# Optimization experiments

Measured on AMD Instinct MI355X. Metric: run time of the kernel, lower is better.

Reference implementation:

```python
import jax, jax.numpy as jnp
import numpy as np

B, S, D = 8, 2048, 1024

def setup_inputs() -> dict:
    key = jax.random.key(0)
    kq, kk, kv = jax.random.split(key, 3)
    qm = jax.random.normal(kq, (B, S, D), dtype=jnp.float32)
    km = jax.random.normal(kk, (B, S, D), dtype=jnp.float32)
    vm = jax.random.normal(kv, (B, S, D), dtype=jnp.float32)
    return {"qm": qm, "km": km, "vm": vm}

def reference(qm, km, vm):
    # qkm = qm @ km^T / sqrt(d_k)   -> [B, S, S]
    scale = 1.0 / jnp.sqrt(jnp.asarray(qm.shape[-1], dtype=qm.dtype))
    qkm = jnp.einsum('bqd,bkd->bqk', qm, km) * scale
    # NOTE: faithful to source: softmax is applied AFTER the second matmul,
    # i.e. softmax((QK^T/sqrt(d)) @ V, axis=-1). masking=False (module default).
    out = jnp.einsum('bqk,bkd->bqd', qkm, vm)  # [B, S, D]
    return jax.nn.softmax(out, axis=-1)
```

## Files before the change

### kernel.cpp

```cpp
#include <hip/hip_runtime.h>
#include <hip/hip_bf16.h>
#include <stdint.h>

#define BATCH 8
#define SEQ   2048
#define DIM   1024

typedef unsigned short u16;
typedef __attribute__((ext_vector_type(8))) short short8;
typedef __attribute__((ext_vector_type(4))) float f32x4;
typedef __attribute__((ext_vector_type(4))) unsigned short us4;

__device__ __forceinline__ u16 f2bf(float x){
  union { float f; uint32_t u; } c; c.f = x;
  uint32_t u = c.u;
  uint32_t r = u + 0x7fffu + ((u >> 16) & 1u);
  return (u16)(r >> 16);
}
__device__ __forceinline__ float bf2f(u16 s){
  union { uint32_t u; float f; } c; c.u = ((uint32_t)s) << 16;
  return c.f;
}

__device__ __forceinline__ void gload16(const void* g, void* l){
  __builtin_amdgcn_global_load_lds(
      (const __attribute__((address_space(1))) void*)g,
      (__attribute__((address_space(3))) void*)l, 16, 0, 0);
}

__global__ __launch_bounds__(256) void k_split(const float* __restrict__ src,
                                               u16* __restrict__ dst, int nchunk){
  for (int i = blockIdx.x*blockDim.x + threadIdx.x; i < nchunk; i += gridDim.x*blockDim.x){
    int r = i >> 8;
    int c = (i & 255) << 2;
    f32x4 v = *(const f32x4*)(src + (size_t)r*DIM + c);
    us4 h, l;
    #pragma unroll
    for (int j = 0; j < 4; j++){
      u16 hh = f2bf(v[j]);
      h[j] = hh;
      l[j] = f2bf(v[j] - bf2f(hh));
    }
    u16* d = dst + (size_t)r*(2*DIM) + c;
    *(us4*)d         = h;
    *(us4*)(d + DIM) = l;
  }
}

__global__ __launch_bounds__(256) void k_convert_kv(const float* __restrict__ K,
                                                    const float* __restrict__ V,
                                                    u16* __restrict__ Kt,
                                                    u16* __restrict__ Vt){
  __shared__ float tile[64][65];
  int z = blockIdx.z;
  const float* Src = (z < 8 ? K : V);
  u16* Dst = (z < 8 ? Kt : Vt);
  int zb = z & 7;
  const float* Vb = Src + (size_t)zb * SEQ * DIM;
  u16* Vtb = Dst + (size_t)zb * DIM * (2*SEQ);
  int s0 = blockIdx.x * 64, d0 = blockIdx.y * 64;
  int t = threadIdx.x;
  int rs = t >> 4;
  int cd = (t & 15) * 4;
  #pragma unroll
  for (int i = 0; i < 4; i++){
    int s = rs + i*16;
    f32x4 v = *(const f32x4*)(Vb + (size_t)(s0 + s)*DIM + d0 + cd);
    tile[s][cd+0] = v[0]; tile[s][cd+1] = v[1];
    tile[s][cd+2] = v[2]; tile[s][cd+3] = v[3];
  }
  __syncthreads();
  int dl = t >> 4;
  int sl = (t & 15) * 4;
  #pragma unroll
  for (int i = 0; i < 4; i++){
    int d = dl + i*16;
    us4 h, l;
    #pragma unroll
    for (int j = 0; j < 4; j++){
      float x = tile[sl+j][d];
      u16 hh = f2bf(x);
      h[j] = hh;
      l[j] = f2bf(x - bf2f(hh));
    }
    size_t off = (size_t)(d0 + d) * (2*SEQ) + s0 + sl;
    *(us4*)(Vtb + off)       = h;
    *(us4*)(Vtb + off + SEQ) = l;
  }
}

template<int KROW, int SPLITK, int TPZX, int TPZY>
__global__ __launch_bounds__(512,1) void k_gemm8(const u16* __restrict__ A,
                                                 const u16* __restrict__ B,
                                                 float* __restrict__ C,
                                                 size_t aStride, size_t bStride, size_t cStride){
  constexpr int LA = 2*KROW;
  constexpr int NT = 1024/32;
  __shared__ __align__(16) u16 lds[2][4][256*32];

  int xcd = blockIdx.x & 7;
  int idx = blockIdx.x >> 3;
  int nPerX = gridDim.x >> 3;
  int gid = xcd * nPerX + idx;
  constexpr int TPZ = TPZX*TPZY;
  int z  = gid / TPZ;
  int rm = gid % TPZ;
  int bx = rm % TPZX;
  int by = rm / TPZX;

  int zb = SPLITK ? (z & 7) : z;
  int kh = SPLITK ? (z >> 3) : 0;

  const u16* Ab = A + (size_t)zb * aStride + (size_t)kh * 1024;
  const u16* Bb = B + (size_t)zb * bStride + (size_t)kh * 1024;
  float* Cb = C + (size_t)z * cStride;

  int t0 = threadIdx.x, lane = t0 & 63, wv = t0 >> 6;
  int wm = (wv >> 2) * 128, wn = (wv & 3) * 64;
  int fr = lane & 15;
  int rdSlot = ((lane >> 4) ^ ((fr >> 1) & 3)) * 8;
  int srow = lane >> 2;
  int srcSlot = ((lane & 3) ^ ((lane >> 3) & 3)) * 8;

  const u16* aB = Ab + ((size_t)bx*256) * LA + srcSlot;
  const u16* bB = Bb + ((size_t)by*256) * LA + srcSlot;
  int ldsB0 = wv*512;

  f32x4 acc[8][4] = {};
  short8 fah[4], fal[4], fbh0[2], fbl0[2], fbh1[2], fbl1[2];

  #define STAGE8(buf, t32)                                                    \
    { _Pragma("unroll")                                                       \
      for (int hf = 0; hf < 2; hf++){                                         \
        size_t ro = (size_t)(wv*16 + hf*128 + srow) * LA + (size_t)(t32)*32;  \
        const u16* ga = aB + ro;                                              \
        const u16* gb = bB + ro;                                              \
        int lo = ldsB0 + hf*4096;                                             \
        gload16(ga,        &lds[buf][0][lo]);                                 \
        gload16(ga + KROW, &lds[buf][1][lo]);                                 \
        gload16(gb,        &lds[buf][2][lo]);                                 \
        gload16(gb + KROW, &lds[buf][3][lo]);                                 \
      } }

  #define LOAD_A(buf, h)                                                      \
    { _Pragma("unroll")                                                       \
      for (int q = 0; q < 4; q++){                                            \
        int ra = (wm + ((h)*4+q)*16 + fr)*32 + rdSlot;                        \
        fah[q] = *(const short8*)&lds[buf][0][ra];                            \
        fal[q] = *(const short8*)&lds[buf][1][ra];                            \
      } }
  #define LOAD_B0(buf)                                                        \
    { _Pragma("unroll")                                                       \
      for (int q = 0; q < 2; q++){                                            \
        int rb = (wn + q*16 + fr)*32 + rdSlot;                                \
        fbh0[q] = *(const short8*)&lds[buf][2][rb];                           \
        fbl0[q] = *(const short8*)&lds[buf][3][rb];                           \
      } }
  #define LOAD_B1(buf)                                                        \
    { _Pragma("unroll")                                                       \
      for (int q = 0; q < 2; q++){                                            \
        int rb = (wn + (2+q)*16 + fr)*32 + rdSlot;                            \
        fbh1[q] = *(const short8*)&lds[buf][2][rb];                           \
        fbl1[q] = *(const short8*)&lds[buf][3][rb];                           \
      } }

  #define MFMA_Q(h, bh, bl, nb)                                               \
    { _Pragma("unroll")                                                       \
      for (int q = 0; q < 4; q++){                                            \
        _Pragma("unroll")                                                     \
        for (int j = 0; j < 2; j++){                                          \
          f32x4 a0 = acc[(h)*4+q][(nb)+j];                                    \
          a0 = __builtin_amdgcn_mfma_f32_16x16x32_bf16(fah[q], bh[j], a0, 0,0,0); \
          a0 = __builtin_amdgcn_mfma_f32_16x16x32_bf16(fah[q], bl[j], a0, 0,0,0); \
          a0 = __builtin_amdgcn_mfma_f32_16x16x32_bf16(fal[q], bh[j], a0, 0,0,0); \
          acc[(h)*4+q][(nb)+j] = a0;                                          \
        } } }

  #define BARR()  __builtin_amdgcn_s_barrier()
  #define LGKM0() { asm volatile("s_waitcnt lgkmcnt(0)" ::: "memory"); __builtin_amdgcn_sched_barrier(0); }
  #define VMC0()  { asm volatile("s_waitcnt vmcnt(0)" ::: "memory"); __builtin_amdgcn_sched_barrier(0); }

  STAGE8(0, 0)
  VMC0()
  BARR();

  for (int t = 0; t < NT; t++){
    int buf = t & 1;
    if (t+1 < NT) STAGE8(buf^1, t+1)
    LOAD_A(buf, 0) LOAD_B0(buf)
    BARR(); LGKM0()
    __builtin_amdgcn_s_setprio(1); MFMA_Q(0, fbh0, fbl0, 0) __builtin_amdgcn_s_setprio(0);
    BARR();
    LOAD_B1(buf)
    BARR(); LGKM0()
    __builtin_amdgcn_s_setprio(1); MFMA_Q(0, fbh1, fbl1, 2) __builtin_amdgcn_s_setprio(0);
    BARR();
    LOAD_A(buf, 1)
    BARR(); LGKM0()
    __builtin_amdgcn_s_setprio(1); MFMA_Q(1, fbh1, fbl1, 2) __builtin_amdgcn_s_setprio(0);
    BARR();
    __builtin_amdgcn_s_setprio(1); MFMA_Q(1, fbh0, fbl0, 0) __builtin_amdgcn_s_setprio(0);
    if (t+1 < NT) VMC0()
    BARR();
  }

  #undef STAGE8
  #undef LOAD_A
  #undef LOAD_B0
  #undef LOAD_B1
  #undef MFMA_Q
  #undef BARR
  #undef LGKM0
  #undef VMC0

  int cr = (lane >> 4) * 4;
  #pragma unroll
  for (int mi = 0; mi < 8; mi++){
    int gr = bx*256 + wm + mi*16 + cr;
    #pragma unroll
    for (int ni = 0; ni < 4; ni++){
      int gc = by*256 + wn + ni*16 + fr;
      #pragma unroll
      for (int e = 0; e < 4; e++)
        Cb[(size_t)(gr + e) * 1024 + gc] = acc[mi][ni][e];
    }
  }
}

__global__ __launch_bounds__(256) void k_reduce_split(const float* __restrict__ P,
                                                      u16* __restrict__ Ws){
  int i = blockIdx.x*256 + threadIdx.x;
  int rg = i >> 8;
  int c  = (i & 255) * 4;
  f32x4 a = *(const f32x4*)(P + (size_t)rg*1024 + c);
  f32x4 b = *(const f32x4*)(P + ((size_t)rg + 8192)*1024 + c);
  us4 h, l;
  #pragma unroll
  for (int j = 0; j < 4; j++){
    float x = (a[j] + b[j]) * 0.03125f;
    u16 hh = f2bf(x);
    h[j] = hh;
    l[j] = f2bf(x - bf2f(hh));
  }
  int zb = rg >> 10, d = rg & 1023;
  u16* Wb = Ws + (size_t)zb * ((size_t)DIM * 2*DIM);
  *(us4*)(Wb + (size_t)d*2048 + c)        = h;
  *(us4*)(Wb + (size_t)d*2048 + 1024 + c) = l;
}

template<int N_, int KB, int SPLITOUT, int BX, int RX, int RY>
__global__ __launch_bounds__(256,2) void k_gemm2ph(const u16* __restrict__ A,
                                                   const u16* __restrict__ B,
                                                   void* __restrict__ Cout,
                                                   size_t aStride, size_t bStride, size_t cStride){
  constexpr int LA = 2*KB;
  __shared__ __align__(16) u16 lds[2][4][128*32];

  int orig = blockIdx.x;
  int xcd = orig & 7;
  int idx = orig >> 3;
  constexpr int RN = RX * RY;
  int z  = idx / RN;
  int r  = idx % RN;
  int bx = (xcd % (BX/RX)) * RX + (r % RX);
  int by = (xcd / (BX/RX)) * RY + (r / RX);

  const u16* Ab = A + (size_t)z * aStride;
  const u16* Bb = B + (size_t)z * bStride;

  int t = threadIdx.x, lane = t & 63, w = t >> 6;
  int wm = (w & 1) * 64, wn = (w >> 1) * 64;
  int fr = lane & 15;
  int srow    = lane >> 2;
  int srcSlot = ((lane & 3) ^ ((lane >> 3) & 3)) * 8;

  const u16* aBase = Ab + ((size_t)bx*128) * LA + srcSlot;
  const u16* bBase = Bb + ((size_t)by*128) * LA + srcSlot;
  int rdSlot = (((lane >> 4) ^ ((fr >> 1) & 3))) * 8;

  f32x4 acc[4][4] = {};

  #define STAGE(buf, k0)                                                      \
    { _Pragma("unroll")                                                       \
      for (int o = 0; o < 2; o++){                                            \
        int c = w*2 + o;                                                      \
        size_t rOff = (size_t)(c*16 + srow) * LA + (k0);                      \
        const u16* ga = aBase + rOff;                                         \
        const u16* gb = bBase + rOff;                                         \
        int le = c * 512;                                                     \
        gload16(ga,      &lds[buf][0][le]);                                   \
        gload16(ga + KB, &lds[buf][1][le]);                                   \
        gload16(gb,      &lds[buf][2][le]);                                   \
        gload16(gb + KB, &lds[buf][3][le]);                                   \
      } }

  #define COMPUTE(buf)                                                        \
    { short8 fah[4], fal[4], fbh[4], fbl[4];                                  \
      _Pragma("unroll")                                                       \
      for (int mi = 0; mi < 4; mi++){                                         \
        fah[mi] = *(const short8*)&lds[buf][0][(wm + mi*16 + fr)*32 + rdSlot];\
        fal[mi] = *(const short8*)&lds[buf][1][(wm + mi*16 + fr)*32 + rdSlot];\
        fbh[mi] = *(const short8*)&lds[buf][2][(wn + mi*16 + fr)*32 + rdSlot];\
        fbl[mi] = *(const short8*)&lds[buf][3][(wn + mi*16 + fr)*32 + rdSlot];\
      }                                                                       \
      _Pragma("unroll")                                                       \
      for (int mi = 0; mi < 4; mi++){                                         \
        _Pragma("unroll")                                                     \
        for (int ni = 0; ni < 4; ni++){                                       \
          acc[mi][ni] = __builtin_amdgcn_mfma_f32_16x16x32_bf16(fah[mi], fbh[ni], acc[mi][ni], 0,0,0); \
          acc[mi][ni] = __builtin_amdgcn_mfma_f32_16x16x32_bf16(fah[mi], fbl[ni], acc[mi][ni], 0,0,0); \
          acc[mi][ni] = __builtin_amdgcn_mfma_f32_16x16x32_bf16(fal[mi], fbh[ni], acc[mi][ni], 0,0,0); \
        }                                                                     \
      } }

  STAGE(0, 0)
  int cur = 0;
  for (int k0 = 0; k0 + 32 < KB; k0 += 32, cur ^= 1){
    STAGE(cur^1, k0 + 32)
    asm volatile("s_waitcnt vmcnt(8)" ::: "memory");
    __builtin_amdgcn_sched_barrier(0);
    __builtin_amdgcn_s_barrier();
    __builtin_amdgcn_sched_barrier(0);
    COMPUTE(cur)
    __builtin_amdgcn_sched_barrier(0);
    __builtin_amdgcn_s_barrier();
  }
  asm volatile("s_waitcnt vmcnt(0)" ::: "memory");
  __builtin_amdgcn_sched_barrier(0);
  __builtin_amdgcn_s_barrier();
  __builtin_amdgcn_sched_barrier(0);
  COMPUTE(cur)

  #undef STAGE
  #undef COMPUTE

  int cr = (lane >> 4) * 4, cc = lane & 15;
  if (SPLITOUT){
    u16* Cb = (u16*)Cout + (size_t)z * cStride;
    const float scale = 0.03125f;
    #pragma unroll
    for (int mi = 0; mi < 4; mi++){
      int gr = bx*128 + wm + mi*16 + cr;
      #pragma unroll
      for (int ni = 0; ni < 4; ni++){
        int gc = by*128 + wn + ni*16 + cc;
        #pragma unroll
        for (int rr = 0; rr < 4; rr++){
          float x = acc[mi][ni][rr] * scale;
          u16 h = f2bf(x);
          u16 l = f2bf(x - bf2f(h));
          size_t off = (size_t)(gr + rr) * (2*N_) + gc;
          Cb[off]      = h;
          Cb[off + N_] = l;
        }
      }
    }
  } else {
    float* Cb = (float*)Cout + (size_t)z * cStride;
    #pragma unroll
    for (int mi = 0; mi < 4; mi++){
      int gr = bx*128 + wm + mi*16 + cr;
      #pragma unroll
      for (int ni = 0; ni < 4; ni++){
        int gc = by*128 + wn + ni*16 + cc;
        #pragma unroll
        for (int rr = 0; rr < 4; rr++){
          Cb[(size_t)(gr + rr) * N_ + gc] = acc[mi][ni][rr];
        }
      }
    }
  }
}

__global__ __launch_bounds__(256) void k_softmax(float* __restrict__ O){
  float* p = O + (size_t)blockIdx.x * DIM;
  int t = threadIdx.x;
  int lane = t & 63, wave = t >> 6;
  f32x4 v = *(f32x4*)(p + t*4);
  float m = fmaxf(fmaxf(v[0], v[1]), fmaxf(v[2], v[3]));
  #pragma unroll
  for (int o = 32; o > 0; o >>= 1) m = fmaxf(m, __shfl_xor(m, o));
  __shared__ float rmax[4], rsum[4];
  if (lane == 0) rmax[wave] = m;
  __syncthreads();
  m = fmaxf(fmaxf(rmax[0], rmax[1]), fmaxf(rmax[2], rmax[3]));
  float e0 = expf(v[0]-m), e1 = expf(v[1]-m), e2 = expf(v[2]-m), e3 = expf(v[3]-m);
  float s = e0 + e1 + e2 + e3;
  #pragma unroll
  for (int o = 32; o > 0; o >>= 1) s += __shfl_xor(s, o);
  if (lane == 0) rsum[wave] = s;
  __syncthreads();
  s = rsum[0] + rsum[1] + rsum[2] + rsum[3];
  float inv = 1.0f / s;
  f32x4 rv = { e0*inv, e1*inv, e2*inv, e3*inv };
  *(f32x4*)(p + t*4) = rv;
}

extern "C" void kernel_launch(void* const* d_in, const int* in_sizes, int n_in,
                              void* d_out, int out_size, void* d_ws, size_t ws_size,
                              hipStream_t stream){
  const float* Q = (const float*)d_in[0];
  const float* K = (const float*)d_in[1];
  const float* V = (const float*)d_in[2];
  float* Out = (float*)d_out;
  u16* w = (u16*)d_ws;

  const size_t QsB = (size_t)SEQ * (2*DIM);
  const size_t KtB = (size_t)DIM * (2*SEQ);
  const size_t VtB = KtB;
  const size_t WsB = (size_t)DIM * (2*DIM);

  dim3 blk(256);
  dim3 cgrid(SEQ/64, DIM/64, 16);

  const size_t base2 = 8 * (KtB + VtB + WsB) * sizeof(u16);
  const size_t needA = base2 + (size_t)16*1024*1024*sizeof(float);
  const size_t needB = base2;

  if (ws_size >= needA){
    u16* Kt = w;
    u16* Vt = Kt + 8*KtB;
    u16* Ws = Vt + 8*VtB;
    float* Part = (float*)(Ws + 8*WsB);
    u16* Qs = w;
    k_convert_kv<<<cgrid, blk, 0, stream>>>(K, V, Kt, Vt);
    k_gemm8<SEQ, 1, 4, 4><<<dim3(256), dim3(512), 0, stream>>>(
        Vt, Kt, Part, VtB, KtB, (size_t)1024*1024);
    k_reduce_split<<<dim3(8192), blk, 0, stream>>>(Part, Ws);
    k_split<<<dim3(2048), blk, 0, stream>>>(Q, Qs, 8*SEQ*(DIM/4));
    k_gemm8<DIM, 0, 8, 4><<<dim3(256), dim3(512), 0, stream>>>(
        Qs, Ws, Out, QsB, WsB, (size_t)SEQ*DIM);
  } else if (ws_size >= needB){
    u16* Kt = w;
    u16* Vt = Kt + 8*KtB;
    u16* Ws = Vt + 8*VtB;
    u16* Qs = w;
    k_convert_kv<<<cgrid, blk, 0, stream>>>(K, V, Kt, Vt);
    k_gemm2ph<DIM, SEQ, 1, 8, 2, 4><<<dim3(512), blk, 0, stream>>>(Vt, Kt, Ws, VtB, KtB, WsB);
    k_split<<<dim3(2048), blk, 0, stream>>>(Q, Qs, 8*SEQ*(DIM/4));
    k_gemm8<DIM, 0, 8, 4><<<dim3(256), dim3(512), 0, stream>>>(
        Qs, Ws, Out, QsB, WsB, (size_t)SEQ*DIM);
  } else {
    u16* Qs = w;
    u16* Kt = Qs + QsB;
    u16* Vt = Kt + KtB;
    u16* Ws = Vt + VtB;
    for (int b = 0; b < BATCH; b++){
      const size_t inOff = (size_t)b * SEQ * DIM;
      k_split<<<dim3(1024), blk, 0, stream>>>(Q + inOff, Qs, SEQ*(DIM/4));
      k_convert_kv<<<dim3(SEQ/64, DIM/64, 1), blk, 0, stream>>>(K + inOff, K + inOff, Kt, Kt);
      k_convert_kv<<<dim3(SEQ/64, DIM/64, 1), blk, 0, stream>>>(V + inOff, V + inOff, Vt, Vt);
      k_gemm2ph<DIM, SEQ, 1, 8, 2, 4><<<dim3(64), blk, 0, stream>>>(Vt, Kt, Ws, VtB, KtB, WsB);
      k_gemm2ph<DIM, DIM, 0, 16, 4, 4><<<dim3(128), blk, 0, stream>>>(Qs, Ws, Out + inOff, QsB, WsB, (size_t)SEQ*DIM);
    }
  }
  k_softmax<<<dim3(BATCH*SEQ), blk, 0, stream>>>(Out);
}
```

Before: 285.4 us.

## Restructure GEMM main loop to cut per-iteration barriers and preload fragments

Rewrites the inner K-loop schedule of the split-bf16 MFMA GEMM. It drops from about eight workgroup barriers and explicit lgkmcnt(0) waits per iteration to two barriers. A partial vmcnt(8) wait lets the next tile's global-to-LDS loads stay in flight while the current tile is consumed. Both B fragment halves are loaded up front, and the second A half goes into its own register set, so the compiler can overlap LDS reads with MFMAs instead of stalling at each barrier. The cost is higher VGPR pressure from the extra fragment registers, which could reduce occupancy or cause spills.

```diff
diff --git a/kernel.cpp b/kernel.cpp
--- a/kernel.cpp
+++ b/kernel.cpp
@@ -127,7 +127,7 @@
   int ldsB0 = wv*512;
 
   f32x4 acc[8][4] = {};
-  short8 fah[4], fal[4], fbh0[2], fbl0[2], fbh1[2], fbl1[2];
+  short8 a0h[4], a0l[4], a1h[4], a1l[4], b0h[2], b0l[2], b1h[2], b1l[2];
 
   #define STAGE8(buf, t32)                                                    \
     { _Pragma("unroll")                                                       \
@@ -142,76 +142,72 @@
         gload16(gb + KROW, &lds[buf][3][lo]);                                 \
       } }
 
-  #define LOAD_A(buf, h)                                                      \
+  #define LOAD_A(buf, h, AH, AL)                                              \
     { _Pragma("unroll")                                                       \
       for (int q = 0; q < 4; q++){                                            \
         int ra = (wm + ((h)*4+q)*16 + fr)*32 + rdSlot;                        \
-        fah[q] = *(const short8*)&lds[buf][0][ra];                            \
-        fal[q] = *(const short8*)&lds[buf][1][ra];                            \
+        AH[q] = *(const short8*)&lds[buf][0][ra];                             \
+        AL[q] = *(const short8*)&lds[buf][1][ra];                             \
       } }
-  #define LOAD_B0(buf)                                                        \
+  #define LOAD_B(buf, nh, BH, BL)                                             \
     { _Pragma("unroll")                                                       \
       for (int q = 0; q < 2; q++){                                            \
-        int rb = (wn + q*16 + fr)*32 + rdSlot;                                \
-        fbh0[q] = *(const short8*)&lds[buf][2][rb];                           \
-        fbl0[q] = *(const short8*)&lds[buf][3][rb];                           \
+        int rb = (wn + ((nh)*2+q)*16 + fr)*32 + rdSlot;                       \
+        BH[q] = *(const short8*)&lds[buf][2][rb];                             \
+        BL[q] = *(const short8*)&lds[buf][3][rb];                             \
       } }
-  #define LOAD_B1(buf)                                                        \
-    { _Pragma("unroll")                                                       \
-      for (int q = 0; q < 2; q++){                                            \
-        int rb = (wn + (2+q)*16 + fr)*32 + rdSlot;                            \
-        fbh1[q] = *(const short8*)&lds[buf][2][rb];                           \
-        fbl1[q] = *(const short8*)&lds[buf][3][rb];                           \
-      } }
-
-  #define MFMA_Q(h, bh, bl, nb)                                               \
+
+  #define MFMA_Q(h, AH, AL, BH, BL, nb)                                       \
     { _Pragma("unroll")                                                       \
       for (int q = 0; q < 4; q++){                                            \
         _Pragma("unroll")                                                     \
         for (int j = 0; j < 2; j++){                                          \
-          f32x4 a0 = acc[(h)*4+q][(nb)+j];                                    \
-          a0 = __builtin_amdgcn_mfma_f32_16x16x32_bf16(fah[q], bh[j], a0, 0,0,0); \
-          a0 = __builtin_amdgcn_mfma_f32_16x16x32_bf16(fah[q], bl[j], a0, 0,0,0); \
-          a0 = __builtin_amdgcn_mfma_f32_16x16x32_bf16(fal[q], bh[j], a0, 0,0,0); \
-          acc[(h)*4+q][(nb)+j] = a0;                                          \
+          f32x4 c0 = acc[(h)*4+q][(nb)+j];                                    \
+          c0 = __builtin_amdgcn_mfma_f32_16x16x32_bf16(AH[q], BH[j], c0, 0,0,0); \
+          c0 = __builtin_amdgcn_mfma_f32_16x16x32_bf16(AH[q], BL[j], c0, 0,0,0); \
+          c0 = __builtin_amdgcn_mfma_f32_16x16x32_bf16(AL[q], BH[j], c0, 0,0,0); \
+          acc[(h)*4+q][(nb)+j] = c0;                                          \
         } } }
 
-  #define BARR()  __builtin_amdgcn_s_barrier()
-  #define LGKM0() { asm volatile("s_waitcnt lgkmcnt(0)" ::: "memory"); __builtin_amdgcn_sched_barrier(0); }
-  #define VMC0()  { asm volatile("s_waitcnt vmcnt(0)" ::: "memory"); __builtin_amdgcn_sched_barrier(0); }
+  #define SB0() __builtin_amdgcn_sched_barrier(0)
 
   STAGE8(0, 0)
-  VMC0()
-  BARR();
+  asm volatile("s_waitcnt vmcnt(0)" ::: "memory");
+  __builtin_amdgcn_s_barrier();
+  SB0();
 
   for (int t = 0; t < NT; t++){
     int buf = t & 1;
-    if (t+1 < NT) STAGE8(buf^1, t+1)
-    LOAD_A(buf, 0) LOAD_B0(buf)
-    BARR(); LGKM0()
-    __builtin_amdgcn_s_setprio(1); MFMA_Q(0, fbh0, fbl0, 0) __builtin_amdgcn_s_setprio(0);
-    BARR();
-    LOAD_B1(buf)
-    BARR(); LGKM0()
-    __builtin_amdgcn_s_setprio(1); MFMA_Q(0, fbh1, fbl1, 2) __builtin_amdgcn_s_setprio(0);
-    BARR();
-    LOAD_A(buf, 1)
-    BARR(); LGKM0()
-    __builtin_amdgcn_s_setprio(1); MFMA_Q(1, fbh1, fbl1, 2) __builtin_amdgcn_s_setprio(0);
-    BARR();
-    __builtin_amdgcn_s_setprio(1); MFMA_Q(1, fbh0, fbl0, 0) __builtin_amdgcn_s_setprio(0);
-    if (t+1 < NT) VMC0()
-    BARR();
+    if (t+1 < NT){
+      STAGE8(buf^1, t+1)
+      asm volatile("s_waitcnt vmcnt(8)" ::: "memory");
+    } else {
+      asm volatile("s_waitcnt vmcnt(0)" ::: "memory");
+    }
+    __builtin_amdgcn_s_barrier();
+    SB0();
+    LOAD_A(buf, 0, a0h, a0l)
+    LOAD_B(buf, 0, b0h, b0l)
+    LOAD_B(buf, 1, b1h, b1l)
+    __builtin_amdgcn_s_setprio(1);
+    MFMA_Q(0, a0h, a0l, b0h, b0l, 0)
+    __builtin_amdgcn_s_setprio(0);
+    LOAD_A(buf, 1, a1h, a1l)
+    __builtin_amdgcn_s_setprio(1);
+    MFMA_Q(0, a0h, a0l, b1h, b1l, 2)
+    MFMA_Q(1, a1h, a1l, b1h, b1l, 2)
+    MFMA_Q(1, a1h, a1l, b0h, b0l, 0)
+    __builtin_amdgcn_s_setprio(0);
+    SB0();
+    __builtin_amdgcn_s_barrier();
+    SB0();
   }
 
   #undef STAGE8
   #undef LOAD_A
-  #undef LOAD_B0
-  #undef LOAD_B1
+  #undef LOAD_B
   #undef MFMA_Q
-  #undef BARR
-  #undef LGKM0
-  #undef VMC0
+  #undef SB0
 
   int cr = (lane >> 4) * 4;
   #pragma unroll
```

Result: no change. 285.5 us (+0.0%).
